# Optimization experiments

Measured on AMD Instinct MI355X. Metric: run time of the kernel, lower is better.

Reference implementation:

```python
import jax, jax.numpy as jnp
import numpy as np

B, A, T, NMODE, H = 4, 16, 32, 8, 256
NSCENE = 512
HEADS = 8
FF = 128
LN_EPS = 1e-6

def _layer_norm(x, g, b, eps=LN_EPS):
    mu = jnp.mean(x, axis=-1, keepdims=True)
    var = jnp.mean((x - mu) ** 2, axis=-1, keepdims=True)
    return (x - mu) * jax.lax.rsqrt(var + eps) * g + b


def setup_inputs() -> dict:
    key = jax.random.key(0)
    ks = jax.random.split(key, 16)
    s = 1.0 / np.sqrt(H)
    sf = 1.0 / np.sqrt(FF)
    return {
        "hidden_vecs": jax.random.normal(ks[0], (B, A, T, NMODE, H), jnp.float32),
        "scene_hidden_vec": jax.random.normal(ks[1], (B, NSCENE, H), jnp.float32),
        # nn.MultiheadAttention packed in_proj: rows [Wq; Wk; Wv]
        "in_proj_w": jax.random.normal(ks[2], (3 * H, H), jnp.float32) * s,
        "in_proj_b": jnp.zeros((3 * H,), jnp.float32),
        "out_proj_w": jax.random.normal(ks[3], (H, H), jnp.float32) * s,
        "out_proj_b": jnp.zeros((H,), jnp.float32),
        "attn_ln_g": jnp.ones((H,), jnp.float32),
        "attn_ln_b": jnp.zeros((H,), jnp.float32),
        "ff1_w": jax.random.normal(ks[4], (FF, H), jnp.float32) * s,
        "ff1_b": jnp.zeros((FF,), jnp.float32),
        "ff2_w": jax.random.normal(ks[5], (H, FF), jnp.float32) * sf,
        "ff2_b": jnp.zeros((H,), jnp.float32),
        "ff_ln_g": jnp.ones((H,), jnp.float32),
        "ff_ln_b": jnp.zeros((H,), jnp.float32),
    }


def reference(hidden_vecs, scene_hidden_vec, in_proj_w, in_proj_b, out_proj_w,
              out_proj_b, attn_ln_g, attn_ln_b, ff1_w, ff1_b, ff2_w, ff2_b,
              ff_ln_g, ff_ln_b):
    b, a, t, n, h = hidden_vecs.shape
    N = scene_hidden_vec.shape[1]
    d = h // HEADS
    m = a * t * n  # queries per batch element

    Wq, Wk, Wv = in_proj_w[:h], in_proj_w[h:2 * h], in_proj_w[2 * h:]
    bq, bk, bv = in_proj_b[:h], in_proj_b[h:2 * h], in_proj_b[2 * h:]

    # Project queries; K/V computed ONCE per batch (shared across a,t,n) --
    # avoids materializing the (b,a,t,n,N,h) expanded tensor.
    q = (hidden_vecs.reshape(b, m, h) @ Wq.T + bq).reshape(b, m, HEADS, d)
    k = (scene_hidden_vec @ Wk.T + bk).reshape(b, N, HEADS, d)
    v = (scene_hidden_vec @ Wv.T + bv).reshape(b, N, HEADS, d)

    scale = 1.0 / np.sqrt(d)
    scores = jnp.einsum('bmed,bned->bemn', q * scale, k)  # (b, heads, m, N)
    attn = jax.nn.softmax(scores, axis=-1)
    ctx = jnp.einsum('bemn,bned->bmed', attn, v).reshape(b, m, h)
    attn_out = (ctx @ out_proj_w.T + out_proj_b).reshape(b, a, t, n, h)

    # averaged attention weights over heads (average_attn_weights=True)
    attn_score = jnp.mean(attn, axis=1).reshape(b, a, t, n, 1, N)

    x = _layer_norm(attn_out + hidden_vecs, attn_ln_g, attn_ln_b)
    ff = jax.nn.relu(x @ ff1_w.T + ff1_b) @ ff2_w.T + ff2_b
    out = _layer_norm(ff + x, ff_ln_g, ff_ln_b)
    return out, attn_score
```

## Files before the change

### kernel.cpp

```cpp
#include <hip/hip_runtime.h>
#include <hip/hip_bf16.h>

#define H 256
#define NSC 512
#define MQ 4096
#define BATCH 4

typedef __attribute__((ext_vector_type(8))) short bf16x8;
typedef __attribute__((ext_vector_type(4))) float f32x4;

__device__ __forceinline__ ushort f2bf(float x) {
    union { float f; unsigned u; } c; c.f = x;
    unsigned r = c.u + 0x7FFF + ((c.u >> 16) & 1);
    return (ushort)(r >> 16);
}
__device__ __forceinline__ unsigned pk2(float hi, float lo) {
    union { float f; unsigned u; } a, b; a.f = hi; b.f = lo;
    return __builtin_amdgcn_perm(a.u, b.u, 0x07060302u);
}
__device__ __forceinline__ uint4 cvt8f(const float* p) {
    float4 a = *(const float4*)p;
    float4 b = *(const float4*)(p + 4);
    uint4 r;
    r.x = pk2(a.y, a.x); r.y = pk2(a.w, a.z);
    r.z = pk2(b.y, b.x); r.w = pk2(b.w, b.z);
    return r;
}
#define EXP2(x) __builtin_amdgcn_exp2f(x)

template<int MODE>
__device__ __forceinline__ void gemm_body(
    ushort* As, ushort* Bs, int bx, int by,
    const float* __restrict__ Ain, const float* __restrict__ W,
    const float* __restrict__ bias,
    void* __restrict__ out, ushort* __restrict__ out2,
    int K, int N, float alpha)
{
    const int t = threadIdx.x;
    const int w = t >> 6, lane = t & 63, g = lane >> 4, l15 = lane & 15;
    const int rowBase = by * 64;
    const int colBase = bx * 256;
    const int wr = (w >> 2) * 32;
    const int wc = (w & 3) * 64;
    f32x4 acc[2][4];
    #pragma unroll
    for (int mt = 0; mt < 2; mt++)
        #pragma unroll
        for (int nt = 0; nt < 4; nt++) acc[mt][nt] = (f32x4){0.f,0.f,0.f,0.f};

    const int sr = t >> 3, skc = t & 7, sp = skc ^ (sr & 7);
    const size_t arow = (size_t)(rowBase + sr) * K + skc * 8;

    uint4 av = cvt8f(Ain + arow);
    uint4 bv[4];
    #pragma unroll
    for (int i = 0; i < 4; i++) {
        const int u = t + 512*i, br = u >> 3, bkc = u & 7;
        int brow = colBase + br; if (brow > N - 1) brow = N - 1;
        bv[i] = cvt8f(W + (size_t)brow * K + bkc*8);
    }

    for (int k0 = 0; k0 < K; k0 += 64) {
        __syncthreads();
        *(uint4*)&As[sr*64 + sp*8] = av;
        #pragma unroll
        for (int i = 0; i < 4; i++) {
            const int u = t + 512*i, br = u >> 3, bkc = u & 7, bp = bkc ^ (br & 7);
            *(uint4*)&Bs[br*64 + bp*8] = bv[i];
        }
        __syncthreads();
        if (k0 + 64 < K) {
            av = cvt8f(Ain + arow + k0 + 64);
            #pragma unroll
            for (int i = 0; i < 4; i++) {
                const int u = t + 512*i, br = u >> 3, bkc = u & 7;
                int brow = colBase + br; if (brow > N - 1) brow = N - 1;
                bv[i] = cvt8f(W + (size_t)brow * K + k0 + 64 + bkc*8);
            }
        }
        #pragma unroll
        for (int kk = 0; kk < 2; kk++) {
            const int swz = ((kk*4 + g) ^ (l15 & 7)) * 8;
            bf16x8 af[2], bfr[4];
            #pragma unroll
            for (int mt = 0; mt < 2; mt++)
                af[mt] = *(const bf16x8*)&As[(wr + mt*16 + l15)*64 + swz];
            #pragma unroll
            for (int nt = 0; nt < 4; nt++)
                bfr[nt] = *(const bf16x8*)&Bs[(wc + nt*16 + l15)*64 + swz];
            #pragma unroll
            for (int mt = 0; mt < 2; mt++)
                #pragma unroll
                for (int nt = 0; nt < 4; nt++)
                    acc[mt][nt] = __builtin_amdgcn_mfma_f32_16x16x32_bf16(
                        af[mt], bfr[nt], acc[mt][nt], 0, 0, 0);
        }
    }

    if (MODE == 0) {
        #pragma unroll
        for (int nt = 0; nt < 4; nt++) {
            const int col = colBase + wc + nt*16 + l15;
            if (col < N) {
                const float bb = bias[col];
                #pragma unroll
                for (int mt = 0; mt < 2; mt++)
                    #pragma unroll
                    for (int r = 0; r < 4; r++) {
                        const int row = rowBase + wr + mt*16 + g*4 + r;
                        float o = (acc[mt][nt][r] + bb) * alpha;
                        ((ushort*)out)[(size_t)row * N + col] = f2bf(o);
                    }
            }
        }
    } else {
        #pragma unroll
        for (int nt = 0; nt < 4; nt++) {
            const int col = colBase + wc + nt*16 + l15;
            const float bb = bias[col];
            #pragma unroll
            for (int mt = 0; mt < 2; mt++) {
                const int row0 = rowBase + wr + mt*16 + g*4;
                if (col < 256) {
                    #pragma unroll
                    for (int r = 0; r < 4; r++)
                        ((ushort*)out)[(size_t)(row0 + r) * 256 + col] = f2bf(acc[mt][nt][r] + bb);
                } else {
                    ushort4 pkv = { f2bf(acc[mt][nt][0] + bb), f2bf(acc[mt][nt][1] + bb),
                                    f2bf(acc[mt][nt][2] + bb), f2bf(acc[mt][nt][3] + bb) };
                    *(ushort4*)&out2[(size_t)((row0 >> 9)*256 + col - 256) * 512 + (row0 & 511)] = pkv;
                }
            }
        }
    }
}

__global__ __launch_bounds__(512, 4) void qkv_kernel(
    const float* __restrict__ hidden, const float* __restrict__ scene,
    const float* __restrict__ in_w, const float* __restrict__ in_b,
    ushort* __restrict__ qb, ushort* __restrict__ kb, ushort* __restrict__ vtb,
    float alpha_q)
{
    __shared__ ushort As[64 * 64];
    __shared__ ushort Bs[256 * 64];
    if (blockIdx.x < 256) {
        gemm_body<0>(As, Bs, 0, blockIdx.x, hidden, in_w, in_b,
                     qb, nullptr, 256, 256, alpha_q);
    } else {
        const int bid = blockIdx.x - 256;
        gemm_body<1>(As, Bs, bid >> 5, bid & 31, scene, in_w + 65536, in_b + 256,
                     kb, vtb, 256, 512, 1.f);
    }
}

__global__ __launch_bounds__(1024, 4) void ffn_kernel(
    const ushort* __restrict__ ctx, const float* __restrict__ Wo,
    const float* __restrict__ bo, const float* __restrict__ hid,
    const float* __restrict__ ag, const float* __restrict__ ab,
    const float* __restrict__ W1, const float* __restrict__ b1,
    const float* __restrict__ W2, const float* __restrict__ b2,
    const float* __restrict__ fg, const float* __restrict__ fbv,
    float* __restrict__ out)
{
    __shared__ ushort As[64 * 64];
    __shared__ ushort Bs[256 * 64];
    __shared__ ushort Xb[64 * 256];
    __shared__ ushort Fb[64 * 128];
    __shared__ float Ls[64 * 4];
    __shared__ float Lq[64 * 4];

    const int t = threadIdx.x;
    const int w = t >> 6, lane = t & 63, g = lane >> 4, l15 = lane & 15;
    const int rowBase = blockIdx.x * 64;
    const int wr = (w >> 2) * 16;
    const int wc = (w & 3) * 64;
    const int sr = t >> 3, skc = t & 7, sp = skc ^ (sr & 7);

    float xres[4][4];

    {
        f32x4 acc[4];
        #pragma unroll
        for (int nt = 0; nt < 4; nt++) acc[nt] = (f32x4){0.f,0.f,0.f,0.f};

        uint4 av;
        if (t < 512) av = *(const uint4*)(ctx + (size_t)(rowBase + sr) * 256 + skc*8);
        uint4 bv[2];
        #pragma unroll
        for (int i = 0; i < 2; i++) {
            const int u = t + 1024*i, br = u >> 3, bkc = u & 7;
            bv[i] = cvt8f(Wo + (size_t)br * 256 + bkc*8);
        }
        for (int k0 = 0; k0 < 256; k0 += 64) {
            __syncthreads();
            if (t < 512) *(uint4*)&As[sr*64 + sp*8] = av;
            #pragma unroll
            for (int i = 0; i < 2; i++) {
                const int u = t + 1024*i, br = u >> 3, bkc = u & 7, bp = bkc ^ (br & 7);
                *(uint4*)&Bs[br*64 + bp*8] = bv[i];
            }
            __syncthreads();
            if (k0 < 192) {
                if (t < 512)
                    av = *(const uint4*)(ctx + (size_t)(rowBase + sr) * 256 + k0 + 64 + skc*8);
                #pragma unroll
                for (int i = 0; i < 2; i++) {
                    const int u = t + 1024*i, br = u >> 3, bkc = u & 7;
                    bv[i] = cvt8f(Wo + (size_t)br * 256 + k0 + 64 + bkc*8);
                }
            }
            #pragma unroll
            for (int kk = 0; kk < 2; kk++) {
                const int swz = ((kk*4 + g) ^ (l15 & 7)) * 8;
                bf16x8 af = *(const bf16x8*)&As[(wr + l15)*64 + swz];
                #pragma unroll
                for (int nt = 0; nt < 4; nt++) {
                    bf16x8 bfr = *(const bf16x8*)&Bs[(wc + nt*16 + l15)*64 + swz];
                    acc[nt] = __builtin_amdgcn_mfma_f32_16x16x32_bf16(
                        af, bfr, acc[nt], 0, 0, 0);
                }
            }
        }
        float bb[4], gmv[4], btv[4];
        #pragma unroll
        for (int nt = 0; nt < 4; nt++) {
            const int col = wc + nt*16 + l15;
            bb[nt] = bo[col]; gmv[nt] = ag[col]; btv[nt] = ab[col];
        }
        #pragma unroll
        for (int r = 0; r < 4; r++) {
            const int row = rowBase + wr + g*4 + r;
            const float* rp = hid + (size_t)row * 256;
            #pragma unroll
            for (int nt = 0; nt < 4; nt++)
                acc[nt][r] += bb[nt] + rp[wc + nt*16 + l15];
        }
        float ps[4], pq[4];
        #pragma unroll
        for (int r = 0; r < 4; r++) {
            float s = (acc[0][r] + acc[1][r]) + (acc[2][r] + acc[3][r]);
            float qq = (acc[0][r]*acc[0][r] + acc[1][r]*acc[1][r])
                     + (acc[2][r]*acc[2][r] + acc[3][r]*acc[3][r]);
            #pragma unroll
            for (int m = 1; m < 16; m <<= 1) {
                s += __shfl_xor(s, m);
                qq += __shfl_xor(qq, m);
            }
            ps[r] = s; pq[r] = qq;
        }
        if (l15 == 0) {
            #pragma unroll
            for (int r = 0; r < 4; r++) {
                const int ri = wr + g*4 + r;
                Ls[ri*4 + (w & 3)] = ps[r];
                Lq[ri*4 + (w & 3)] = pq[r];
            }
        }
        __syncthreads();
        #pragma unroll
        for (int r = 0; r < 4; r++) {
            const int ri = wr + g*4 + r;
            f32x4 sv = *(const f32x4*)&Ls[ri*4];
            f32x4 qv = *(const f32x4*)&Lq[ri*4];
            const float mu = (sv[0]+sv[1]+sv[2]+sv[3]) * (1.f/256.f);
            const float ex2 = (qv[0]+qv[1]+qv[2]+qv[3]) * (1.f/256.f);
            const float rs = rsqrtf(ex2 - mu*mu + 1e-6f);
            #pragma unroll
            for (int nt = 0; nt < 4; nt++) {
                const int col = wc + nt*16 + l15;
                const float o = (acc[nt][r] - mu) * rs * gmv[nt] + btv[nt];
                xres[nt][r] = o;
                Xb[ri*256 + (((col >> 3) ^ (ri & 7)) << 3) + (col & 7)] = f2bf(o);
            }
        }
    }

    {
        const int wrB = (w >> 2) * 16;
        const int wcB = (w & 3) * 32;
        f32x4 facc[2];
        #pragma unroll
        for (int nt = 0; nt < 2; nt++) facc[nt] = (f32x4){0.f,0.f,0.f,0.f};

        uint4 bv2 = cvt8f(W1 + (size_t)(t >> 3) * 256 + (t & 7)*8);
        for (int k0 = 0; k0 < 256; k0 += 64) {
            __syncthreads();
            {
                const int br = t >> 3, bkc = t & 7, bp = bkc ^ (br & 7);
                *(uint4*)&Bs[br*64 + bp*8] = bv2;
            }
            __syncthreads();
            if (k0 < 192)
                bv2 = cvt8f(W1 + (size_t)(t >> 3) * 256 + k0 + 64 + (t & 7)*8);
            #pragma unroll
            for (int kk = 0; kk < 2; kk++) {
                const int rowX = wrB + l15;
                const int gi = (k0 >> 3) + kk*4 + g;
                bf16x8 af = *(const bf16x8*)&Xb[rowX*256 + ((gi ^ (rowX & 7)) << 3)];
                const int swz = ((kk*4 + g) ^ (l15 & 7)) * 8;
                #pragma unroll
                for (int nt = 0; nt < 2; nt++) {
                    bf16x8 bfr = *(const bf16x8*)&Bs[(wcB + nt*16 + l15)*64 + swz];
                    facc[nt] = __builtin_amdgcn_mfma_f32_16x16x32_bf16(
                        af, bfr, facc[nt], 0, 0, 0);
                }
            }
        }
        #pragma unroll
        for (int nt = 0; nt < 2; nt++) {
            const int colF = wcB + nt*16 + l15;
            const float fbb = b1[colF];
            #pragma unroll
            for (int r = 0; r < 4; r++) {
                const int rowF = wrB + g*4 + r;
                const float o = fmaxf(facc[nt][r] + fbb, 0.f);
                Fb[rowF*128 + (((colF >> 3) ^ (rowF & 7)) << 3) + (colF & 7)] = f2bf(o);
            }
        }
        __syncthreads();
    }

    {
        f32x4 acc2[4];
        #pragma unroll
        for (int nt = 0; nt < 4; nt++) acc2[nt] = (f32x4){0.f,0.f,0.f,0.f};

        uint4 bv3[2];
        #pragma unroll
        for (int i = 0; i < 2; i++) {
            const int u = t + 1024*i, br = u >> 3, bkc = u & 7;
            bv3[i] = cvt8f(W2 + (size_t)br * 128 + bkc*8);
        }
        for (int k0 = 0; k0 < 128; k0 += 64) {
            __syncthreads();
            #pragma unroll
            for (int i = 0; i < 2; i++) {
                const int u = t + 1024*i, br = u >> 3, bkc = u & 7, bp = bkc ^ (br & 7);
                *(uint4*)&Bs[br*64 + bp*8] = bv3[i];
            }
            __syncthreads();
            if (k0 == 0) {
                #pragma unroll
                for (int i = 0; i < 2; i++) {
                    const int u = t + 1024*i, br = u >> 3, bkc = u & 7;
                    bv3[i] = cvt8f(W2 + (size_t)br * 128 + 64 + bkc*8);
                }
            }
            #pragma unroll
            for (int kk = 0; kk < 2; kk++) {
                const int gi = (k0 >> 3) + kk*4 + g;
                const int rowF = wr + l15;
                bf16x8 af2 = *(const bf16x8*)&Fb[rowF*128 + ((gi ^ (rowF & 7)) << 3)];
                const int swz = ((kk*4 + g) ^ (l15 & 7)) * 8;
                #pragma unroll
                for (int nt = 0; nt < 4; nt++) {
                    bf16x8 bfr = *(const bf16x8*)&Bs[(wc + nt*16 + l15)*64 + swz];
                    acc2[nt] = __builtin_amdgcn_mfma_f32_16x16x32_bf16(
                        af2, bfr, acc2[nt], 0, 0, 0);
                }
            }
        }
        float bb[4], gmv[4], btv[4];
        #pragma unroll
        for (int nt = 0; nt < 4; nt++) {
            const int col = wc + nt*16 + l15;
            bb[nt] = b2[col]; gmv[nt] = fg[col]; btv[nt] = fbv[col];
        }
        #pragma unroll
        for (int r = 0; r < 4; r++)
            #pragma unroll
            for (int nt = 0; nt < 4; nt++)
                acc2[nt][r] += bb[nt] + xres[nt][r];
        float ps[4], pq[4];
        #pragma unroll
        for (int r = 0; r < 4; r++) {
            float s = (acc2[0][r] + acc2[1][r]) + (acc2[2][r] + acc2[3][r]);
            float qq = (acc2[0][r]*acc2[0][r] + acc2[1][r]*acc2[1][r])
                     + (acc2[2][r]*acc2[2][r] + acc2[3][r]*acc2[3][r]);
            #pragma unroll
            for (int m = 1; m < 16; m <<= 1) {
                s += __shfl_xor(s, m);
                qq += __shfl_xor(qq, m);
            }
            ps[r] = s; pq[r] = qq;
        }
        __syncthreads();
        if (l15 == 0) {
            #pragma unroll
            for (int r = 0; r < 4; r++) {
                const int ri = wr + g*4 + r;
                Ls[ri*4 + (w & 3)] = ps[r];
                Lq[ri*4 + (w & 3)] = pq[r];
            }
        }
        __syncthreads();
        #pragma unroll
        for (int r = 0; r < 4; r++) {
            const int ri = wr + g*4 + r;
            const int row = rowBase + ri;
            f32x4 sv = *(const f32x4*)&Ls[ri*4];
            f32x4 qv = *(const f32x4*)&Lq[ri*4];
            const float mu = (sv[0]+sv[1]+sv[2]+sv[3]) * (1.f/256.f);
            const float ex2 = (qv[0]+qv[1]+qv[2]+qv[3]) * (1.f/256.f);
            const float rs = rsqrtf(ex2 - mu*mu + 1e-6f);
            #pragma unroll
            for (int nt = 0; nt < 4; nt++) {
                const int col = wc + nt*16 + l15;
                out[(size_t)row * 256 + col] =
                    (acc2[nt][r] - mu) * rs * gmv[nt] + btv[nt];
            }
        }
    }
}

__global__ __launch_bounds__(512, 4) void attn_kernel(
    const ushort* __restrict__ q, const ushort* __restrict__ k,
    const ushort* __restrict__ vt, ushort* __restrict__ ctx_out,
    float* __restrict__ attn_score)
{
    __shared__ ushort Ks[32 * 264];
    __shared__ ushort Vs[256 * 40];
    __shared__ ushort Pb[8 * 32 * 40];
    __shared__ float Lg[256];
    const int t = threadIdx.x;
    const int w = t >> 6;
    const int lane = t & 63;
    const int g = lane >> 4;
    const int l15 = lane & 15;
    const int b = blockIdx.x >> 7;
    const int m0 = (blockIdx.x & 127) * 32;

    const size_t kg = (size_t)b * NSC * H;
    const size_t vg = (size_t)b * H * NSC;

    bf16x8 qf[2];
    #pragma unroll
    for (int qt = 0; qt < 2; qt++)
        qf[qt] = *(const bf16x8*)&q[((size_t)(b*MQ + m0 + qt*16 + l15)) * H + w*32 + g*8];

    f32x4 cacc[2][2];
    float lacc[2][4];
    #pragma unroll
    for (int qt = 0; qt < 2; qt++) {
        #pragma unroll
        for (int dt = 0; dt < 2; dt++) cacc[qt][dt] = (f32x4){0.f,0.f,0.f,0.f};
        #pragma unroll
        for (int r = 0; r < 4; r++) lacc[qt][r] = 0.f;
    }

    bf16x8 kr[2], vr[2];
    #pragma unroll
    for (int i = 0; i < 2; i++) {
        const int u = t + 512*i;
        const int key = u >> 5, part = u & 31;
        kr[i] = *(const bf16x8*)&k[kg + (size_t)key*H + part*8];
        const int d = u >> 2, p2 = u & 3;
        vr[i] = *(const bf16x8*)&vt[vg + (size_t)d*NSC + p2*8];
    }

    for (int c = 0; c < 16; c++) {
        const int kbase = c * 32;
        __syncthreads();
        #pragma unroll
        for (int i = 0; i < 2; i++) {
            const int u = t + 512*i;
            const int key = u >> 5, part = u & 31;
            *(bf16x8*)&Ks[key*264 + part*8] = kr[i];
            const int d = u >> 2, p2 = u & 3;
            *(bf16x8*)&Vs[d*40 + p2*8] = vr[i];
        }
        __syncthreads();
        if (c < 15) {
            #pragma unroll
            for (int i = 0; i < 2; i++) {
                const int u = t + 512*i;
                const int key = u >> 5, part = u & 31;
                kr[i] = *(const bf16x8*)&k[kg + (size_t)(kbase + 32 + key)*H + part*8];
                const int d = u >> 2, p2 = u & 3;
                vr[i] = *(const bf16x8*)&vt[vg + (size_t)d*NSC + kbase + 32 + p2*8];
            }
        }
        #pragma unroll
        for (int qt = 0; qt < 2; qt++) {
            #pragma unroll
            for (int kt = 0; kt < 2; kt++) {
                bf16x8 kf = *(const bf16x8*)&Ks[(kt*16 + l15)*264 + w*32 + g*8];
                f32x4 s = __builtin_amdgcn_mfma_f32_16x16x32_bf16(
                    qf[qt], kf, (f32x4){0.f,0.f,0.f,0.f}, 0, 0, 0);
                #pragma unroll
                for (int r = 0; r < 4; r++) {
                    float p = EXP2(s[r]);
                    lacc[qt][r] += p;
                    Pb[(w*32 + qt*16 + g*4 + r)*40 + kt*16 + l15] = f2bf(p);
                }
            }
        }
        #pragma unroll
        for (int qt = 0; qt < 2; qt++) {
            bf16x8 pf = *(const bf16x8*)&Pb[(w*32 + qt*16 + l15)*40 + g*8];
            #pragma unroll
            for (int dt = 0; dt < 2; dt++) {
                bf16x8 vf = *(const bf16x8*)&Vs[(w*32 + dt*16 + l15)*40 + g*8];
                cacc[qt][dt] = __builtin_amdgcn_mfma_f32_16x16x32_bf16(
                    pf, vf, cacc[qt][dt], 0, 0, 0);
            }
        }
    }

    #pragma unroll
    for (int qt = 0; qt < 2; qt++) {
        float invl[4];
        #pragma unroll
        for (int r = 0; r < 4; r++) {
            float v = lacc[qt][r];
            v += __shfl_xor(v, 1); v += __shfl_xor(v, 2);
            v += __shfl_xor(v, 4); v += __shfl_xor(v, 8);
            invl[r] = 1.f / v;
            if (l15 == 0) Lg[w*32 + qt*16 + g*4 + r] = -__log2f(v) - 3.0f;
        }
        #pragma unroll
        for (int dt = 0; dt < 2; dt++)
            #pragma unroll
            for (int r = 0; r < 4; r++)
                ctx_out[((size_t)(b*MQ + m0 + qt*16 + g*4 + r))*H + w*32 + dt*16 + l15]
                    = f2bf(cacc[qt][dt][r] * invl[r]);
    }

    __syncthreads();

    f32x4 sacc[2][4];
    #pragma unroll
    for (int qt = 0; qt < 2; qt++)
        #pragma unroll
        for (int kt = 0; kt < 4; kt++) sacc[qt][kt] = (f32x4){0.f,0.f,0.f,0.f};

    #pragma unroll 2
    for (int h = 0; h < 8; h++) {
        const float lg0 = Lg[h*32 + l15];
        const float lg1 = Lg[h*32 + 16 + l15];
        bf16x8 q0 = *(const bf16x8*)&q[((size_t)(b*MQ + m0 + l15)) * H + h*32 + g*8];
        bf16x8 q1 = *(const bf16x8*)&q[((size_t)(b*MQ + m0 + 16 + l15)) * H + h*32 + g*8];
        #pragma unroll
        for (int kt = 0; kt < 4; kt++) {
            bf16x8 kf = *(const bf16x8*)&k[kg + (size_t)(w*64 + kt*16 + l15)*H + h*32 + g*8];
            f32x4 s0 = __builtin_amdgcn_mfma_f32_16x16x32_bf16(
                kf, q0, (f32x4){0.f,0.f,0.f,0.f}, 0, 0, 0);
            #pragma unroll
            for (int r = 0; r < 4; r++) sacc[0][kt][r] += EXP2(s0[r] + lg0);
            f32x4 s1 = __builtin_amdgcn_mfma_f32_16x16x32_bf16(
                kf, q1, (f32x4){0.f,0.f,0.f,0.f}, 0, 0, 0);
            #pragma unroll
            for (int r = 0; r < 4; r++) sacc[1][kt][r] += EXP2(s1[r] + lg1);
        }
    }
    #pragma unroll
    for (int qt = 0; qt < 2; qt++)
        #pragma unroll
        for (int kt = 0; kt < 4; kt++)
            *(f32x4*)&attn_score[((size_t)(b*MQ + m0 + qt*16 + l15))*NSC + w*64 + kt*16 + g*4]
                = sacc[qt][kt];
}

extern "C" void kernel_launch(void* const* d_in, const int* in_sizes, int n_in,
                              void* d_out, int out_size, void* d_ws, size_t ws_size,
                              hipStream_t stream)
{
    const float* hidden = (const float*)d_in[0];
    const float* scene  = (const float*)d_in[1];
    const float* in_w   = (const float*)d_in[2];
    const float* in_b   = (const float*)d_in[3];
    const float* out_w  = (const float*)d_in[4];
    const float* out_b  = (const float*)d_in[5];
    const float* aln_g  = (const float*)d_in[6];
    const float* aln_b  = (const float*)d_in[7];
    const float* ff1_w  = (const float*)d_in[8];
    const float* ff1_b  = (const float*)d_in[9];
    const float* ff2_w  = (const float*)d_in[10];
    const float* ff2_b  = (const float*)d_in[11];
    const float* fln_g  = (const float*)d_in[12];
    const float* fln_b  = (const float*)d_in[13];

    float* out0  = (float*)d_out;
    float* score = out0 + (size_t)BATCH * MQ * H;

    ushort* qb   = (ushort*)d_ws;
    ushort* kb   = qb   + 4194304;
    ushort* vtb  = kb   + 524288;
    ushort* ctxb = vtb  + 524288;

    const float alpha_q = 0.25507609683638066f;

    qkv_kernel<<<dim3(320), dim3(512), 0, stream>>>(
        hidden, scene, in_w, in_b, qb, kb, vtb, alpha_q);
    attn_kernel<<<dim3(512), dim3(512), 0, stream>>>(qb, kb, vtb, ctxb, score);
    ffn_kernel<<<dim3(256), dim3(1024), 0, stream>>>(
        ctxb, out_w, out_b, hidden, aln_g, aln_b,
        ff1_w, ff1_b, ff2_w, ff2_b, fln_g, fln_b, out0);
}
```

Measured before the change: 185.0 us.

## Load K/V MFMA fragments directly from global, dropping LDS staging and barriers

The attention kernel no longer stages K and V chunks through shared memory. Each wave now loads its own per-head K and V fragments straight from global memory into registers, prefetching the next chunk one iteration ahead. This removes two block-wide __syncthreads per chunk and cuts LDS usage, which may allow more blocks per CU. In exchange, global loads are strided row fragments instead of coalesced tile loads, so the kernel relies on L2/L1 hits. The per-wave Pb buffer now depends on wave-local ordering rather than block barriers.

```diff
diff --git a/kernel.cpp b/kernel.cpp
--- a/kernel.cpp
+++ b/kernel.cpp
@@ -418,8 +418,6 @@
     const ushort* __restrict__ vt, ushort* __restrict__ ctx_out,
     float* __restrict__ attn_score)
 {
-    __shared__ ushort Ks[32 * 264];
-    __shared__ ushort Vs[256 * 40];
     __shared__ ushort Pb[8 * 32 * 40];
     __shared__ float Lg[256];
     const int t = threadIdx.x;
@@ -448,45 +446,31 @@
         for (int r = 0; r < 4; r++) lacc[qt][r] = 0.f;
     }
 
-    bf16x8 kr[2], vr[2];
-    #pragma unroll
-    for (int i = 0; i < 2; i++) {
-        const int u = t + 512*i;
-        const int key = u >> 5, part = u & 31;
-        kr[i] = *(const bf16x8*)&k[kg + (size_t)key*H + part*8];
-        const int d = u >> 2, p2 = u & 3;
-        vr[i] = *(const bf16x8*)&vt[vg + (size_t)d*NSC + p2*8];
-    }
+    bf16x8 kf[2], vf[2];
+    #pragma unroll
+    for (int kt = 0; kt < 2; kt++)
+        kf[kt] = *(const bf16x8*)&k[kg + (size_t)(kt*16 + l15)*H + w*32 + g*8];
+    #pragma unroll
+    for (int dt = 0; dt < 2; dt++)
+        vf[dt] = *(const bf16x8*)&vt[vg + (size_t)(w*32 + dt*16 + l15)*NSC + g*8];
 
     for (int c = 0; c < 16; c++) {
         const int kbase = c * 32;
-        __syncthreads();
-        #pragma unroll
-        for (int i = 0; i < 2; i++) {
-            const int u = t + 512*i;
-            const int key = u >> 5, part = u & 31;
-            *(bf16x8*)&Ks[key*264 + part*8] = kr[i];
-            const int d = u >> 2, p2 = u & 3;
-            *(bf16x8*)&Vs[d*40 + p2*8] = vr[i];
-        }
-        __syncthreads();
-        if (c < 15) {
-            #pragma unroll
-            for (int i = 0; i < 2; i++) {
-                const int u = t + 512*i;
-                const int key = u >> 5, part = u & 31;
-                kr[i] = *(const bf16x8*)&k[kg + (size_t)(kbase + 32 + key)*H + part*8];
-                const int d = u >> 2, p2 = u & 3;
-                vr[i] = *(const bf16x8*)&vt[vg + (size_t)d*NSC + kbase + 32 + p2*8];
-            }
-        }
+        const int nbase = (c < 15) ? kbase + 32 : kbase;
+        bf16x8 kn[2], vn[2];
+        #pragma unroll
+        for (int kt = 0; kt < 2; kt++)
+            kn[kt] = *(const bf16x8*)&k[kg + (size_t)(nbase + kt*16 + l15)*H + w*32 + g*8];
+        #pragma unroll
+        for (int dt = 0; dt < 2; dt++)
+            vn[dt] = *(const bf16x8*)&vt[vg + (size_t)(w*32 + dt*16 + l15)*NSC + nbase + g*8];
+
         #pragma unroll
         for (int qt = 0; qt < 2; qt++) {
             #pragma unroll
             for (int kt = 0; kt < 2; kt++) {
-                bf16x8 kf = *(const bf16x8*)&Ks[(kt*16 + l15)*264 + w*32 + g*8];
                 f32x4 s = __builtin_amdgcn_mfma_f32_16x16x32_bf16(
-                    qf[qt], kf, (f32x4){0.f,0.f,0.f,0.f}, 0, 0, 0);
+                    qf[qt], kf[kt], (f32x4){0.f,0.f,0.f,0.f}, 0, 0, 0);
                 #pragma unroll
                 for (int r = 0; r < 4; r++) {
                     float p = EXP2(s[r]);
@@ -499,12 +483,12 @@
         for (int qt = 0; qt < 2; qt++) {
             bf16x8 pf = *(const bf16x8*)&Pb[(w*32 + qt*16 + l15)*40 + g*8];
             #pragma unroll
-            for (int dt = 0; dt < 2; dt++) {
-                bf16x8 vf = *(const bf16x8*)&Vs[(w*32 + dt*16 + l15)*40 + g*8];
+            for (int dt = 0; dt < 2; dt++)
                 cacc[qt][dt] = __builtin_amdgcn_mfma_f32_16x16x32_bf16(
-                    pf, vf, cacc[qt][dt], 0, 0, 0);
-            }
-        }
+                    pf, vf[dt], cacc[qt][dt], 0, 0, 0);
+        }
+        kf[0] = kn[0]; kf[1] = kn[1];
+        vf[0] = vn[0]; vf[1] = vn[1];
     }
 
     #pragma unroll
@@ -542,13 +526,13 @@
         bf16x8 q1 = *(const bf16x8*)&q[((size_t)(b*MQ + m0 + 16 + l15)) * H + h*32 + g*8];
         #pragma unroll
         for (int kt = 0; kt < 4; kt++) {
-            bf16x8 kf = *(const bf16x8*)&k[kg + (size_t)(w*64 + kt*16 + l15)*H + h*32 + g*8];
+            bf16x8 kf2 = *(const bf16x8*)&k[kg + (size_t)(w*64 + kt*16 + l15)*H + h*32 + g*8];
             f32x4 s0 = __builtin_amdgcn_mfma_f32_16x16x32_bf16(
-                kf, q0, (f32x4){0.f,0.f,0.f,0.f}, 0, 0, 0);
+                kf2, q0, (f32x4){0.f,0.f,0.f,0.f}, 0, 0, 0);
             #pragma unroll
             for (int r = 0; r < 4; r++) sacc[0][kt][r] += EXP2(s0[r] + lg0);
             f32x4 s1 = __builtin_amdgcn_mfma_f32_16x16x32_bf16(
-                kf, q1, (f32x4){0.f,0.f,0.f,0.f}, 0, 0, 0);
+                kf2, q1, (f32x4){0.f,0.f,0.f,0.f}, 0, 0, 0);
             #pragma unroll
             for (int r = 0; r < 4; r++) sacc[1][kt][r] += EXP2(s1[r] + lg1);
         }
```

After: 197.9 us. 7.0% more time.

## Fuse attention kernel into FFN kernel, keeping context in shared memory

Applied to the files above, without the earlier changes.

Merges the attention kernel and the out-proj/FFN kernel into one 1024-thread kernel that handles 64 query rows per block. The context tile stays in LDS for the output projection instead of being written to global memory as bf16 and read back. Shared memory is reused across phases through one aliased buffer. The costs are fewer blocks (256 instead of 512 for the attention phase), larger per-block LDS use, and possibly lower occupancy.

```diff
diff --git a/kernel.cpp b/kernel.cpp
--- a/kernel.cpp
+++ b/kernel.cpp
@@ -153,38 +153,163 @@
     }
 }
 
-__global__ __launch_bounds__(1024, 4) void ffn_kernel(
-    const ushort* __restrict__ ctx, const float* __restrict__ Wo,
-    const float* __restrict__ bo, const float* __restrict__ hid,
+__global__ __launch_bounds__(1024, 4) void mega_kernel(
+    const ushort* __restrict__ q, const ushort* __restrict__ k,
+    const ushort* __restrict__ vt,
+    const float* __restrict__ Wo, const float* __restrict__ bo,
+    const float* __restrict__ hid,
     const float* __restrict__ ag, const float* __restrict__ ab,
     const float* __restrict__ W1, const float* __restrict__ b1,
     const float* __restrict__ W2, const float* __restrict__ b2,
     const float* __restrict__ fg, const float* __restrict__ fbv,
-    float* __restrict__ out)
+    float* __restrict__ out, float* __restrict__ attn_score)
 {
-    __shared__ ushort As[64 * 64];
-    __shared__ ushort Bs[256 * 64];
-    __shared__ ushort Xb[64 * 256];
-    __shared__ ushort Fb[64 * 128];
-    __shared__ float Ls[64 * 4];
-    __shared__ float Lq[64 * 4];
+    __shared__ uint4 SHraw[8096];
+    ushort* SH = (ushort*)SHraw;
+    ushort* Ks = SH;
+    ushort* Vs = SH + 8448;
+    ushort* Pb = SH + 18688;
+    ushort* Cb = SH + 39168;
+    float*  Lg = (float*)(SH + 63744);
+    ushort* Bs = SH;
+    ushort* Xb = SH + 18688;
+    float*  Ls = (float*)(SH + 35072);
+    float*  Lq = (float*)(SH + 35584);
+    ushort* Fb = SH + 55552;
 
     const int t = threadIdx.x;
     const int w = t >> 6, lane = t & 63, g = lane >> 4, l15 = lane & 15;
-    const int rowBase = blockIdx.x * 64;
+    const int b = blockIdx.x >> 6;
+    const int m0 = (blockIdx.x & 63) * 64;
+    const size_t rowG = (size_t)b * MQ + m0;
+    const size_t kg = (size_t)b * NSC * H;
+    const size_t vg = (size_t)b * H * NSC;
+
+    const int hh0 = w & 7, hf = w >> 3;
+    bf16x8 qf[2];
+    #pragma unroll
+    for (int qt = 0; qt < 2; qt++)
+        qf[qt] = *(const bf16x8*)&q[(rowG + hf*32 + qt*16 + l15) * H + hh0*32 + g*8];
+
+    f32x4 cacc[2][2];
+    float lacc[2][4];
+    #pragma unroll
+    for (int qt = 0; qt < 2; qt++) {
+        #pragma unroll
+        for (int dt = 0; dt < 2; dt++) cacc[qt][dt] = (f32x4){0.f,0.f,0.f,0.f};
+        #pragma unroll
+        for (int r = 0; r < 4; r++) lacc[qt][r] = 0.f;
+    }
+
+    const int skey = t >> 5, spart = t & 31;
+    const int sd = t >> 2, sp2 = t & 3;
+    bf16x8 kr = *(const bf16x8*)&k[kg + (size_t)skey*H + spart*8];
+    bf16x8 vr = *(const bf16x8*)&vt[vg + (size_t)sd*NSC + sp2*8];
+
+    for (int c = 0; c < 16; c++) {
+        const int kbase = c * 32;
+        __syncthreads();
+        *(bf16x8*)&Ks[skey*264 + spart*8] = kr;
+        *(bf16x8*)&Vs[sd*40 + sp2*8] = vr;
+        __syncthreads();
+        if (c < 15) {
+            kr = *(const bf16x8*)&k[kg + (size_t)(kbase + 32 + skey)*H + spart*8];
+            vr = *(const bf16x8*)&vt[vg + (size_t)sd*NSC + kbase + 32 + sp2*8];
+        }
+        #pragma unroll
+        for (int qt = 0; qt < 2; qt++) {
+            #pragma unroll
+            for (int kt = 0; kt < 2; kt++) {
+                bf16x8 kf = *(const bf16x8*)&Ks[(kt*16 + l15)*264 + hh0*32 + g*8];
+                f32x4 s = __builtin_amdgcn_mfma_f32_16x16x32_bf16(
+                    qf[qt], kf, (f32x4){0.f,0.f,0.f,0.f}, 0, 0, 0);
+                #pragma unroll
+                for (int r = 0; r < 4; r++) {
+                    float p = EXP2(s[r]);
+                    lacc[qt][r] += p;
+                    Pb[(w*32 + qt*16 + g*4 + r)*40 + kt*16 + l15] = f2bf(p);
+                }
+            }
+        }
+        #pragma unroll
+        for (int qt = 0; qt < 2; qt++) {
+            bf16x8 pf = *(const bf16x8*)&Pb[(w*32 + qt*16 + l15)*40 + g*8];
+            #pragma unroll
+            for (int dt = 0; dt < 2; dt++) {
+                bf16x8 vf = *(const bf16x8*)&Vs[(hh0*32 + dt*16 + l15)*40 + g*8];
+                cacc[qt][dt] = __builtin_amdgcn_mfma_f32_16x16x32_bf16(
+                    pf, vf, cacc[qt][dt], 0, 0, 0);
+            }
+        }
+    }
+
+    #pragma unroll
+    for (int qt = 0; qt < 2; qt++) {
+        float invl[4];
+        #pragma unroll
+        for (int r = 0; r < 4; r++) {
+            float v = lacc[qt][r];
+            v += __shfl_xor(v, 1); v += __shfl_xor(v, 2);
+            v += __shfl_xor(v, 4); v += __shfl_xor(v, 8);
+            invl[r] = 1.f / v;
+            if (l15 == 0) Lg[hh0*64 + hf*32 + qt*16 + g*4 + r] = -__log2f(v) - 3.0f;
+        }
+        #pragma unroll
+        for (int dt = 0; dt < 2; dt++)
+            #pragma unroll
+            for (int r = 0; r < 4; r++) {
+                const int qr = hf*32 + qt*16 + g*4 + r;
+                const int col = hh0*32 + dt*16 + l15;
+                Cb[qr*256 + (((col >> 3) ^ (qr & 7)) << 3) + (col & 7)]
+                    = f2bf(cacc[qt][dt][r] * invl[r]);
+            }
+    }
+
+    __syncthreads();
+
+    {
+        f32x4 sacc[4][2];
+        #pragma unroll
+        for (int qt = 0; qt < 4; qt++)
+            #pragma unroll
+            for (int kt = 0; kt < 2; kt++) sacc[qt][kt] = (f32x4){0.f,0.f,0.f,0.f};
+
+        #pragma unroll 2
+        for (int h = 0; h < 8; h++) {
+            float lgq[4]; bf16x8 qv[4];
+            #pragma unroll
+            for (int qt = 0; qt < 4; qt++) {
+                lgq[qt] = Lg[h*64 + qt*16 + l15];
+                qv[qt] = *(const bf16x8*)&q[(rowG + qt*16 + l15) * H + h*32 + g*8];
+            }
+            #pragma unroll
+            for (int kt = 0; kt < 2; kt++) {
+                bf16x8 kf2 = *(const bf16x8*)&k[kg + (size_t)(w*32 + kt*16 + l15)*H + h*32 + g*8];
+                #pragma unroll
+                for (int qt = 0; qt < 4; qt++) {
+                    f32x4 s = __builtin_amdgcn_mfma_f32_16x16x32_bf16(
+                        kf2, qv[qt], (f32x4){0.f,0.f,0.f,0.f}, 0, 0, 0);
+                    #pragma unroll
+                    for (int r = 0; r < 4; r++) sacc[qt][kt][r] += EXP2(s[r] + lgq[qt]);
+                }
+            }
+        }
+        #pragma unroll
+        for (int qt = 0; qt < 4; qt++)
+            #pragma unroll
+            for (int kt = 0; kt < 2; kt++)
+                *(f32x4*)&attn_score[(rowG + qt*16 + l15)*NSC + w*32 + kt*16 + g*4]
+                    = sacc[qt][kt];
+    }
+
     const int wr = (w >> 2) * 16;
     const int wc = (w & 3) * 64;
-    const int sr = t >> 3, skc = t & 7, sp = skc ^ (sr & 7);
-
     float xres[4][4];
-
     {
         f32x4 acc[4];
         #pragma unroll
         for (int nt = 0; nt < 4; nt++) acc[nt] = (f32x4){0.f,0.f,0.f,0.f};
 
-        uint4 av;
-        if (t < 512) av = *(const uint4*)(ctx + (size_t)(rowBase + sr) * 256 + skc*8);
         uint4 bv[2];
         #pragma unroll
         for (int i = 0; i < 2; i++) {
@@ -193,7 +318,6 @@
         }
         for (int k0 = 0; k0 < 256; k0 += 64) {
             __syncthreads();
-            if (t < 512) *(uint4*)&As[sr*64 + sp*8] = av;
             #pragma unroll
             for (int i = 0; i < 2; i++) {
                 const int u = t + 1024*i, br = u >> 3, bkc = u & 7, bp = bkc ^ (br & 7);
@@ -201,8 +325,6 @@
             }
             __syncthreads();
             if (k0 < 192) {
-                if (t < 512)
-                    av = *(const uint4*)(ctx + (size_t)(rowBase + sr) * 256 + k0 + 64 + skc*8);
                 #pragma unroll
                 for (int i = 0; i < 2; i++) {
                     const int u = t + 1024*i, br = u >> 3, bkc = u & 7;
@@ -211,8 +333,10 @@
             }
             #pragma unroll
             for (int kk = 0; kk < 2; kk++) {
+                const int rowC = wr + l15;
+                const int gi = (k0 >> 3) + kk*4 + g;
+                bf16x8 af = *(const bf16x8*)&Cb[rowC*256 + ((gi ^ (rowC & 7)) << 3)];
                 const int swz = ((kk*4 + g) ^ (l15 & 7)) * 8;
-                bf16x8 af = *(const bf16x8*)&As[(wr + l15)*64 + swz];
                 #pragma unroll
                 for (int nt = 0; nt < 4; nt++) {
                     bf16x8 bfr = *(const bf16x8*)&Bs[(wc + nt*16 + l15)*64 + swz];
@@ -229,8 +353,7 @@
         }
         #pragma unroll
         for (int r = 0; r < 4; r++) {
-            const int row = rowBase + wr + g*4 + r;
-            const float* rp = hid + (size_t)row * 256;
+            const float* rp = hid + (rowG + wr + g*4 + r) * 256;
             #pragma unroll
             for (int nt = 0; nt < 4; nt++)
                 acc[nt][r] += bb[nt] + rp[wc + nt*16 + l15];
@@ -261,9 +384,9 @@
         for (int r = 0; r < 4; r++) {
             const int ri = wr + g*4 + r;
             f32x4 sv = *(const f32x4*)&Ls[ri*4];
-            f32x4 qv = *(const f32x4*)&Lq[ri*4];
+            f32x4 qv2 = *(const f32x4*)&Lq[ri*4];
             const float mu = (sv[0]+sv[1]+sv[2]+sv[3]) * (1.f/256.f);
-            const float ex2 = (qv[0]+qv[1]+qv[2]+qv[3]) * (1.f/256.f);
+            const float ex2 = (qv2[0]+qv2[1]+qv2[2]+qv2[3]) * (1.f/256.f);
             const float rs = rsqrtf(ex2 - mu*mu + 1e-6f);
             #pragma unroll
             for (int nt = 0; nt < 4; nt++) {
@@ -397,168 +520,19 @@
         #pragma unroll
         for (int r = 0; r < 4; r++) {
             const int ri = wr + g*4 + r;
-            const int row = rowBase + ri;
             f32x4 sv = *(const f32x4*)&Ls[ri*4];
-            f32x4 qv = *(const f32x4*)&Lq[ri*4];
+            f32x4 qv2 = *(const f32x4*)&Lq[ri*4];
             const float mu = (sv[0]+sv[1]+sv[2]+sv[3]) * (1.f/256.f);
-            const float ex2 = (qv[0]+qv[1]+qv[2]+qv[3]) * (1.f/256.f);
+            const float ex2 = (qv2[0]+qv2[1]+qv2[2]+qv2[3]) * (1.f/256.f);
             const float rs = rsqrtf(ex2 - mu*mu + 1e-6f);
             #pragma unroll
             for (int nt = 0; nt < 4; nt++) {
                 const int col = wc + nt*16 + l15;
-                out[(size_t)row * 256 + col] =
+                out[(rowG + ri) * 256 + col] =
                     (acc2[nt][r] - mu) * rs * gmv[nt] + btv[nt];
             }
         }
     }
-}
-
-__global__ __launch_bounds__(512, 4) void attn_kernel(
-    const ushort* __restrict__ q, const ushort* __restrict__ k,
-    const ushort* __restrict__ vt, ushort* __restrict__ ctx_out,
-    float* __restrict__ attn_score)
-{
-    __shared__ ushort Ks[32 * 264];
-    __shared__ ushort Vs[256 * 40];
-    __shared__ ushort Pb[8 * 32 * 40];
-    __shared__ float Lg[256];
-    const int t = threadIdx.x;
-    const int w = t >> 6;
-    const int lane = t & 63;
-    const int g = lane >> 4;
-    const int l15 = lane & 15;
-    const int b = blockIdx.x >> 7;
-    const int m0 = (blockIdx.x & 127) * 32;
-
-    const size_t kg = (size_t)b * NSC * H;
-    const size_t vg = (size_t)b * H * NSC;
-
-    bf16x8 qf[2];
-    #pragma unroll
-    for (int qt = 0; qt < 2; qt++)
-        qf[qt] = *(const bf16x8*)&q[((size_t)(b*MQ + m0 + qt*16 + l15)) * H + w*32 + g*8];
-
-    f32x4 cacc[2][2];
-    float lacc[2][4];
-    #pragma unroll
-    for (int qt = 0; qt < 2; qt++) {
-        #pragma unroll
-        for (int dt = 0; dt < 2; dt++) cacc[qt][dt] = (f32x4){0.f,0.f,0.f,0.f};
-        #pragma unroll
-        for (int r = 0; r < 4; r++) lacc[qt][r] = 0.f;
-    }
-
-    bf16x8 kr[2], vr[2];
-    #pragma unroll
-    for (int i = 0; i < 2; i++) {
-        const int u = t + 512*i;
-        const int key = u >> 5, part = u & 31;
-        kr[i] = *(const bf16x8*)&k[kg + (size_t)key*H + part*8];
-        const int d = u >> 2, p2 = u & 3;
-        vr[i] = *(const bf16x8*)&vt[vg + (size_t)d*NSC + p2*8];
-    }
-
-    for (int c = 0; c < 16; c++) {
-        const int kbase = c * 32;
-        __syncthreads();
-        #pragma unroll
-        for (int i = 0; i < 2; i++) {
-            const int u = t + 512*i;
-            const int key = u >> 5, part = u & 31;
-            *(bf16x8*)&Ks[key*264 + part*8] = kr[i];
-            const int d = u >> 2, p2 = u & 3;
-            *(bf16x8*)&Vs[d*40 + p2*8] = vr[i];
-        }
-        __syncthreads();
-        if (c < 15) {
-            #pragma unroll
-            for (int i = 0; i < 2; i++) {
-                const int u = t + 512*i;
-                const int key = u >> 5, part = u & 31;
-                kr[i] = *(const bf16x8*)&k[kg + (size_t)(kbase + 32 + key)*H + part*8];
-                const int d = u >> 2, p2 = u & 3;
-                vr[i] = *(const bf16x8*)&vt[vg + (size_t)d*NSC + kbase + 32 + p2*8];
-            }
-        }
-        #pragma unroll
-        for (int qt = 0; qt < 2; qt++) {
-            #pragma unroll
-            for (int kt = 0; kt < 2; kt++) {
-                bf16x8 kf = *(const bf16x8*)&Ks[(kt*16 + l15)*264 + w*32 + g*8];
-                f32x4 s = __builtin_amdgcn_mfma_f32_16x16x32_bf16(
-                    qf[qt], kf, (f32x4){0.f,0.f,0.f,0.f}, 0, 0, 0);
-                #pragma unroll
-                for (int r = 0; r < 4; r++) {
-                    float p = EXP2(s[r]);
-                    lacc[qt][r] += p;
-                    Pb[(w*32 + qt*16 + g*4 + r)*40 + kt*16 + l15] = f2bf(p);
-                }
-            }
-        }
-        #pragma unroll
-        for (int qt = 0; qt < 2; qt++) {
-            bf16x8 pf = *(const bf16x8*)&Pb[(w*32 + qt*16 + l15)*40 + g*8];
-            #pragma unroll
-            for (int dt = 0; dt < 2; dt++) {
-                bf16x8 vf = *(const bf16x8*)&Vs[(w*32 + dt*16 + l15)*40 + g*8];
-                cacc[qt][dt] = __builtin_amdgcn_mfma_f32_16x16x32_bf16(
-                    pf, vf, cacc[qt][dt], 0, 0, 0);
-            }
-        }
-    }
-
-    #pragma unroll
-    for (int qt = 0; qt < 2; qt++) {
-        float invl[4];
-        #pragma unroll
-        for (int r = 0; r < 4; r++) {
-            float v = lacc[qt][r];
-            v += __shfl_xor(v, 1); v += __shfl_xor(v, 2);
-            v += __shfl_xor(v, 4); v += __shfl_xor(v, 8);
-            invl[r] = 1.f / v;
-            if (l15 == 0) Lg[w*32 + qt*16 + g*4 + r] = -__log2f(v) - 3.0f;
-        }
-        #pragma unroll
-        for (int dt = 0; dt < 2; dt++)
-            #pragma unroll
-            for (int r = 0; r < 4; r++)
-                ctx_out[((size_t)(b*MQ + m0 + qt*16 + g*4 + r))*H + w*32 + dt*16 + l15]
-                    = f2bf(cacc[qt][dt][r] * invl[r]);
-    }
-
-    __syncthreads();
-
-    f32x4 sacc[2][4];
-    #pragma unroll
-    for (int qt = 0; qt < 2; qt++)
-        #pragma unroll
-        for (int kt = 0; kt < 4; kt++) sacc[qt][kt] = (f32x4){0.f,0.f,0.f,0.f};
-
-    #pragma unroll 2
-    for (int h = 0; h < 8; h++) {
-        const float lg0 = Lg[h*32 + l15];
-        const float lg1 = Lg[h*32 + 16 + l15];
-        bf16x8 q0 = *(const bf16x8*)&q[((size_t)(b*MQ + m0 + l15)) * H + h*32 + g*8];
-        bf16x8 q1 = *(const bf16x8*)&q[((size_t)(b*MQ + m0 + 16 + l15)) * H + h*32 + g*8];
-        #pragma unroll
-        for (int kt = 0; kt < 4; kt++) {
-            bf16x8 kf = *(const bf16x8*)&k[kg + (size_t)(w*64 + kt*16 + l15)*H + h*32 + g*8];
-            f32x4 s0 = __builtin_amdgcn_mfma_f32_16x16x32_bf16(
-                kf, q0, (f32x4){0.f,0.f,0.f,0.f}, 0, 0, 0);
-            #pragma unroll
-            for (int r = 0; r < 4; r++) sacc[0][kt][r] += EXP2(s0[r] + lg0);
-            f32x4 s1 = __builtin_amdgcn_mfma_f32_16x16x32_bf16(
-                kf, q1, (f32x4){0.f,0.f,0.f,0.f}, 0, 0, 0);
-            #pragma unroll
-            for (int r = 0; r < 4; r++) sacc[1][kt][r] += EXP2(s1[r] + lg1);
-        }
-    }
-    #pragma unroll
-    for (int qt = 0; qt < 2; qt++)
-        #pragma unroll
-        for (int kt = 0; kt < 4; kt++)
-            *(f32x4*)&attn_score[((size_t)(b*MQ + m0 + qt*16 + l15))*NSC + w*64 + kt*16 + g*4]
-                = sacc[qt][kt];
 }
 
 extern "C" void kernel_launch(void* const* d_in, const int* in_sizes, int n_in,
@@ -586,14 +560,14 @@
     ushort* qb   = (ushort*)d_ws;
     ushort* kb   = qb   + 4194304;
     ushort* vtb  = kb   + 524288;
-    ushort* ctxb = vtb  + 524288;
 
     const float alpha_q = 0.25507609683638066f;
 
     qkv_kernel<<<dim3(320), dim3(512), 0, stream>>>(
         hidden, scene, in_w, in_b, qb, kb, vtb, alpha_q);
-    attn_kernel<<<dim3(512), dim3(512), 0, stream>>>(qb, kb, vtb, ctxb, score);
-    ffn_kernel<<<dim3(256), dim3(1024), 0, stream>>>(
-        ctxb, out_w, out_b, hidden, aln_g, aln_b,
-        ff1_w, ff1_b, ff2_w, ff2_b, fln_g, fln_b, out0);
-}
+    mega_kernel<<<dim3(256), dim3(1024), 0, stream>>>(
+        qb, kb, vtb,
+        out_w, out_b, hidden, aln_g, aln_b,
+        ff1_w, ff1_b, ff2_w, ff2_b, fln_g, fln_b,
+        out0, score);
+}
```

Result: faster. 179.4 us (-3.0%).
